# Performance work log

Hardware: AMD Instinct MI355X
Metric: run time of the kernel (lower is better)

The kernel has to match this reference:

```python
import jax, jax.numpy as jnp
import numpy as np

S, D, H = 4096, 2048, 16
HD = D // H

def setup_inputs() -> dict:
    key = jax.random.key(0)
    ks = jax.random.split(key, 9)
    s = 1.0 / np.sqrt(D)
    return {
        "hidden_states": jax.random.normal(ks[0], (S, D), jnp.float32),
        "Wq": jax.random.uniform(ks[1], (D, D), jnp.float32, -s, s),
        "bq": jax.random.uniform(ks[2], (D,), jnp.float32, -s, s),
        "Wk": jax.random.uniform(ks[3], (D, D), jnp.float32, -s, s),
        "bk": jax.random.uniform(ks[4], (D,), jnp.float32, -s, s),
        "Wv": jax.random.uniform(ks[5], (D, D), jnp.float32, -s, s),
        "bv": jax.random.uniform(ks[6], (D,), jnp.float32, -s, s),
        "Wo": jax.random.uniform(ks[7], (D, D), jnp.float32, -s, s),
        "bo": jax.random.uniform(ks[8], (D,), jnp.float32, -s, s),
    }

def reference(hidden_states, Wq, bq, Wk, bk, Wv, bv, Wo, bo):
    seq = hidden_states.shape[0]
    # projections (torch Linear: x @ W.T + b)
    q = (hidden_states @ Wq.T + bq).reshape(seq, H, HD).transpose(1, 0, 2)  # [H,S,hd]
    k = (hidden_states @ Wk.T + bk).reshape(seq, H, HD).transpose(1, 0, 2)
    v = (hidden_states @ Wv.T + bv).reshape(seq, H, HD).transpose(1, 0, 2)
    scale = 1.0 / np.sqrt(HD).astype(np.float32)
    qk = jnp.einsum('hqd,hkd->hqk', q, k) * scale  # [H,S,S]
    causal = jnp.tril(jnp.ones((seq, seq), bool))
    qk = jnp.where(causal, qk, -jnp.inf)
    attn = jax.nn.softmax(qk, axis=-1)
    out = jnp.einsum('hqk,hkd->hqd', attn, v)  # [H,S,hd]
    out = out.transpose(1, 0, 2).reshape(seq, D)
    return out @ Wo.T + bo
```

## Files before the change

### kernel.cpp

```cpp
#include <hip/hip_runtime.h>
#include <stdint.h>

#define S_LEN 4096
#define D_DIM 2048
#define NHEAD 16
#define HDIM  128

typedef short bf16x8 __attribute__((ext_vector_type(8)));
typedef float f32x4  __attribute__((ext_vector_type(4)));
typedef float f32x16 __attribute__((ext_vector_type(16)));

__device__ __forceinline__ unsigned short f2bf(float x) {
  union { float f; unsigned u; } v; v.f = x;
  unsigned r = v.u + 0x7FFFu + ((v.u >> 16) & 1u);
  return (unsigned short)(r >> 16);
}

__device__ __forceinline__ float bf2f(unsigned short s) {
  union { unsigned u; float f; } v; v.u = ((unsigned)s) << 16;
  return v.f;
}

__device__ __forceinline__ unsigned cvtpk_bf16(float lo, float hi_) {
  unsigned r;
  asm("v_cvt_pk_bf16_f32 %0, %1, %2" : "=v"(r) : "v"(lo), "v"(hi_));
  return r;
}

__device__ __forceinline__ void gload_lds16(const void* g, void* l) {
  __builtin_amdgcn_global_load_lds(
      (const __attribute__((address_space(1))) unsigned int*)g,
      (__attribute__((address_space(3))) unsigned int*)l, 16, 0, 0);
}

__global__ __launch_bounds__(256) void cvt_all(
    const float* __restrict__ X, const float* __restrict__ Wq,
    const float* __restrict__ Wk, const float* __restrict__ Wv,
    const float* __restrict__ Wo, unsigned short* __restrict__ out) {
  const size_t DD = (size_t)D_DIM * D_DIM;
  size_t i = ((size_t)blockIdx.x * 256 + threadIdx.x) * 8;
  const float* src; size_t off;
  if (i < 2 * DD)      { src = X;  off = i; }
  else if (i < 3 * DD) { src = Wq; off = i - 2 * DD; }
  else if (i < 4 * DD) { src = Wk; off = i - 3 * DD; }
  else if (i < 5 * DD) { src = Wv; off = i - 4 * DD; }
  else                 { src = Wo; off = i - 5 * DD; }
  float4 a = *(const float4*)(src + off);
  float4 b = *(const float4*)(src + off + 4);
  union { unsigned short s[8]; bf16x8 v; } o;
  o.s[0] = f2bf(a.x); o.s[1] = f2bf(a.y); o.s[2] = f2bf(a.z); o.s[3] = f2bf(a.w);
  o.s[4] = f2bf(b.x); o.s[5] = f2bf(b.y); o.s[6] = f2bf(b.z); o.s[7] = f2bf(b.w);
  *(bf16x8*)(out + i) = o.v;
}

__device__ __forceinline__ void stage256(
    const unsigned short* __restrict__ A, const unsigned short* __restrict__ W,
    unsigned short* la, unsigned short* lb, int m0, int n0, int k0,
    int wv, int lane) {
  const int K = 2048;
#pragma unroll
  for (int p = 0; p < 4; ++p) {
    const int off = wv * 1024 + p * 8192;
    const int o = off + lane * 16;
    const int half = o >> 14, rowh = (o >> 7) & 127, ch = (o >> 4) & 7;
    const int row = half * 128 + rowh;
    const int csrc = (ch ^ (rowh & 7)) * 8;
    gload_lds16(A + (size_t)(m0 + row) * K + k0 + csrc, la + (off >> 1));
    gload_lds16(W + (size_t)(n0 + row) * K + k0 + csrc, lb + (off >> 1));
  }
}

__global__ __launch_bounds__(512, 1) void gemm_qkv2(
    const unsigned short* __restrict__ A, const unsigned short* __restrict__ W,
    const float* __restrict__ bq, const float* __restrict__ bk,
    const float* __restrict__ bv, unsigned short* __restrict__ Q,
    unsigned short* __restrict__ Ko, unsigned short* __restrict__ V,
    float qsc) {
  __shared__ __attribute__((aligned(16))) unsigned short LA[2][16384];
  __shared__ __attribute__((aligned(16))) unsigned short LB[2][16384];
  const int m0 = blockIdx.y * 256, n0 = blockIdx.x * 256;
  const int tid = threadIdx.x, lane = tid & 63, wv = tid >> 6;
  const int wm = wv >> 2, wn = wv & 3;
  const int rA = lane & 15, g4 = lane >> 4;

  f32x4 acc[8][4];
#pragma unroll
  for (int i = 0; i < 8; ++i)
#pragma unroll
    for (int j = 0; j < 4; ++j)
#pragma unroll
      for (int r = 0; r < 4; ++r) acc[i][j][r] = 0.f;

  stage256(A, W, &LA[0][0], &LB[0][0], m0, n0, 0, wv, lane);
  stage256(A, W, &LA[1][0], &LB[1][0], m0, n0, 64, wv, lane);
  asm volatile("s_waitcnt vmcnt(8)" ::: "memory");
  __builtin_amdgcn_s_barrier();
  __builtin_amdgcn_sched_barrier(0);

  for (int t = 0; t < 32; ++t) {
    const unsigned short* la = &LA[t & 1][0] + wm * 8192;
    const unsigned short* lb = &LB[t & 1][0] + (wn >> 1) * 8192;
    const int rbB = (wn & 1) * 64;
#pragma unroll
    for (int kk = 0; kk < 2; ++kk) {
      bf16x8 af[8], bfv[4];
      const int sw = ((kk * 4 + g4) ^ (rA & 7)) * 8;
#pragma unroll
      for (int i = 0; i < 8; ++i)
        af[i] = *(const bf16x8*)(la + (i * 16 + rA) * 64 + sw);
#pragma unroll
      for (int j = 0; j < 4; ++j)
        bfv[j] = *(const bf16x8*)(lb + (rbB + j * 16 + rA) * 64 + sw);
      __builtin_amdgcn_s_setprio(1);
#pragma unroll
      for (int i = 0; i < 8; ++i)
#pragma unroll
        for (int j = 0; j < 4; ++j)
          acc[i][j] = __builtin_amdgcn_mfma_f32_16x16x32_bf16(af[i], bfv[j], acc[i][j], 0, 0, 0);
      __builtin_amdgcn_s_setprio(0);
    }
    if (t == 31) break;
    __builtin_amdgcn_s_barrier();
    __builtin_amdgcn_sched_barrier(0);
    if (t + 2 < 32) {
      stage256(A, W, &LA[t & 1][0], &LB[t & 1][0], m0, n0, (t + 2) * 64, wv, lane);
      asm volatile("s_waitcnt vmcnt(8)" ::: "memory");
    } else {
      asm volatile("s_waitcnt vmcnt(0)" ::: "memory");
    }
    __builtin_amdgcn_s_barrier();
    __builtin_amdgcn_sched_barrier(0);
  }

  const int cR = g4 * 4, cC = rA;
  const int seg = n0 >> 11;
  const float* bp = (seg == 0) ? bq : (seg == 1) ? bk : bv;
  unsigned short* op = (seg == 0) ? Q : (seg == 1) ? Ko : V;
  const float es = (seg == 0) ? qsc : 1.0f;
  const int ncl0 = (n0 & 2047) + wn * 64;
#pragma unroll
  for (int j = 0; j < 4; ++j) {
    const int col = ncl0 + j * 16 + cC;
    const float bvv = bp[col];
#pragma unroll
    for (int i = 0; i < 8; ++i) {
      const int row0 = m0 + wm * 128 + i * 16 + cR;
#pragma unroll
      for (int r = 0; r < 4; ++r)
        op[(size_t)(row0 + r) * D_DIM + col] = f2bf((acc[i][j][r] + bvv) * es);
    }
  }
}

__global__ __launch_bounds__(256, 2) void gemm_bt_f32(
    const unsigned short* __restrict__ A, const unsigned short* __restrict__ B,
    const float* __restrict__ bias, float* __restrict__ Cout,
    int M, int N, int K) {
  __shared__ __attribute__((aligned(16))) unsigned short As[128 * 32];
  __shared__ __attribute__((aligned(16))) unsigned short Bs[128 * 32];
  const int m0 = blockIdx.y * 128, n0 = blockIdx.x * 128;
  const int tid = threadIdx.x, lane = tid & 63, wv = tid >> 6;
  const int wm = wv >> 1, wn = wv & 1;
  const int rA = lane & 15, kb = (lane >> 4) * 8;

  f32x4 acc[4][4];
#pragma unroll
  for (int i = 0; i < 4; ++i)
#pragma unroll
    for (int j = 0; j < 4; ++j)
#pragma unroll
      for (int r = 0; r < 4; ++r) acc[i][j][r] = 0.f;

  for (int k0 = 0; k0 < K; k0 += 32) {
    __syncthreads();
#pragma unroll
    for (int p = 0; p < 2; ++p) {
      const int rr = (wv * 2 + p) * 16 + (lane >> 2);
      const int cc = lane & 3;
      gload_lds16(A + (size_t)(m0 + rr) * K + k0 + cc * 8, As + (wv * 2 + p) * 512);
      gload_lds16(B + (size_t)(n0 + rr) * K + k0 + cc * 8, Bs + (wv * 2 + p) * 512);
    }
    __syncthreads();
    bf16x8 af[4], bfr[4];
#pragma unroll
    for (int i = 0; i < 4; ++i)
      af[i] = *(const bf16x8*)(As + (wm * 64 + i * 16 + rA) * 32 + kb);
#pragma unroll
    for (int j = 0; j < 4; ++j)
      bfr[j] = *(const bf16x8*)(Bs + (wn * 64 + j * 16 + rA) * 32 + kb);
#pragma unroll
    for (int i = 0; i < 4; ++i)
#pragma unroll
      for (int j = 0; j < 4; ++j)
        acc[i][j] = __builtin_amdgcn_mfma_f32_16x16x32_bf16(af[i], bfr[j], acc[i][j], 0, 0, 0);
  }

  const int cR = (lane >> 4) * 4, cC = lane & 15;
#pragma unroll
  for (int j = 0; j < 4; ++j) {
    const int col = n0 + wn * 64 + j * 16 + cC;
    const float bvv = bias[col];
#pragma unroll
    for (int i = 0; i < 4; ++i) {
      const int row0 = m0 + wm * 64 + i * 16 + cR;
#pragma unroll
      for (int r = 0; r < 4; ++r)
        Cout[(size_t)(row0 + r) * N + col] = acc[i][j][r] + bvv;
    }
  }
}

__global__ __launch_bounds__(256, 2) void attn_part(
    const unsigned short* __restrict__ Qb, const unsigned short* __restrict__ Kb,
    const unsigned short* __restrict__ Vb, unsigned short* __restrict__ Opart,
    float* __restrict__ ML) {
  __shared__ __attribute__((aligned(16))) unsigned short Ks[64 * 128];
  __shared__ __attribute__((aligned(16))) unsigned short Vt[128 * 64];
  const int bid = blockIdx.x;
  const int h  = ((bid & 7) << 1) | ((bid >> 3) & 1);
  const int hf = (bid >> 4) & 1;
  const int qi = 31 - (bid >> 5);
  const int q0 = qi * 128;
  const int u2 = (h * 32 + qi) * 2 + hf;
  const int tid = threadIdx.x, lane = tid & 63, wv = tid >> 6;
  const int qc = lane & 31, hi = lane >> 5;
  const int q0w = q0 + wv * 32;
  const int myq = q0w + qc;
  const int kp = tid & 31, hb = (tid >> 5) * 16;

  bf16x8 qf[8];
#pragma unroll
  for (int sl = 0; sl < 8; ++sl)
    qf[sl] = *(const bf16x8*)(Qb + (size_t)myq * D_DIM + h * HDIM + sl * 16 + hi * 8);

  f32x16 oacc[4];
#pragma unroll
  for (int nf = 0; nf < 4; ++nf)
#pragma unroll
    for (int r = 0; r < 16; ++r) oacc[nf][r] = 0.f;
  float mh = -3.0e38f, l = 0.f;

  const int klo = hf * (qi + 1), khi = klo + qi + 1;
  const int wqmax = q0w + 31;

  for (int kt = klo; kt < khi; ++kt) {
    const int k0 = kt * 64;
    __syncthreads();
#pragma unroll
    for (int p = 0; p < 4; ++p) {
      const int ob = wv * 4096 + p * 1024;
      const int o = ob + lane * 16;
      const int r = o >> 8, c = (o >> 4) & 15;
      gload_lds16(Kb + (size_t)(k0 + r) * D_DIM + h * HDIM + (c ^ (r & 7)) * 8,
                  Ks + ob / 2);
    }
    {
      const unsigned short* s0 = Vb + (size_t)(k0 + 2 * kp) * D_DIM + h * HDIM + hb;
      union { uint4 u[4]; unsigned short s[32]; } t;
      t.u[0] = *(const uint4*)s0;           t.u[1] = *(const uint4*)(s0 + 8);
      t.u[2] = *(const uint4*)(s0 + D_DIM); t.u[3] = *(const uint4*)(s0 + D_DIM + 8);
#pragma unroll
      for (int w = 0; w < 16; ++w) {
        const int hd = hb + w;
        const unsigned val = (unsigned)t.s[w] | ((unsigned)t.s[16 + w] << 16);
        *(unsigned*)((char*)Vt + hd * 128 + (((kp >> 2) ^ (hd & 7)) << 4) + ((kp & 3) << 2)) = val;
      }
    }
    __syncthreads();
    if (k0 > wqmax) continue;

    f32x16 sacc[2];
#pragma unroll
    for (int kb = 0; kb < 2; ++kb)
#pragma unroll
      for (int r = 0; r < 16; ++r) sacc[kb][r] = 0.f;
    __builtin_amdgcn_s_setprio(1);
#pragma unroll
    for (int sl = 0; sl < 8; ++sl) {
#pragma unroll
      for (int kb = 0; kb < 2; ++kb) {
        const int row = kb * 32 + qc;
        bf16x8 kfr = *(const bf16x8*)((const char*)Ks + row * 256 +
                                      (((2 * sl + hi) ^ (qc & 7)) << 4));
        sacc[kb] = __builtin_amdgcn_mfma_f32_32x32x16_bf16(kfr, qf[sl], sacc[kb], 0, 0, 0);
      }
    }
    __builtin_amdgcn_s_setprio(0);

    const bool needmask = (k0 + 63 > q0w);
    if (needmask) {
      const int dq = myq - k0;
#pragma unroll
      for (int kb = 0; kb < 2; ++kb)
#pragma unroll
        for (int r = 0; r < 16; ++r) {
          const int kk = kb * 32 + (r & 3) + 8 * (r >> 2) + 4 * hi;
          if (kk > dq) sacc[kb][r] = -3.0e38f;
        }
    }
    float mx0[8];
#pragma unroll
    for (int t = 0; t < 8; ++t)
      mx0[t] = fmaxf(fmaxf(sacc[0][t], sacc[0][t + 8]),
                     fmaxf(sacc[1][t], sacc[1][t + 8]));
    float mx = fmaxf(fmaxf(fmaxf(mx0[0], mx0[1]), fmaxf(mx0[2], mx0[3])),
                     fmaxf(fmaxf(mx0[4], mx0[5]), fmaxf(mx0[6], mx0[7])));
    mx = fmaxf(mx, __shfl_xor(mx, 32));
    if (!__all(mx <= mh + 11.5f)) {
      const float mnew = fmaxf(mh, mx);
      const float corr = exp2f(mh - mnew);
      mh = mnew;
      l *= corr;
#pragma unroll
      for (int r = 0; r < 16; ++r) {
        const float cr = __shfl(corr, (r & 3) + 8 * (r >> 2) + 4 * hi);
#pragma unroll
        for (int nf = 0; nf < 4; ++nf) oacc[nf][r] *= cr;
      }
    }
    float rs = 0.f;
#pragma unroll
    for (int kb = 0; kb < 2; ++kb)
#pragma unroll
      for (int r = 0; r < 16; ++r) {
        const float p = exp2f(sacc[kb][r] - mh);
        sacc[kb][r] = p;
        rs += p;
      }
    rs += __shfl_xor(rs, 32);
    l += rs;

    bf16x8 pa[4];
#pragma unroll
    for (int kb = 0; kb < 2; ++kb)
#pragma unroll
      for (int s = 0; s < 2; ++s) {
        const int b = s * 8;
        unsigned pk0 = cvtpk_bf16(sacc[kb][b + 0], sacc[kb][b + 1]);
        unsigned pk1 = cvtpk_bf16(sacc[kb][b + 2], sacc[kb][b + 3]);
        unsigned pk2 = cvtpk_bf16(sacc[kb][b + 4], sacc[kb][b + 5]);
        unsigned pk3 = cvtpk_bf16(sacc[kb][b + 6], sacc[kb][b + 7]);
        const unsigned sw0 = (unsigned)__shfl_xor((int)pk0, 32);
        const unsigned sw1 = (unsigned)__shfl_xor((int)pk1, 32);
        const unsigned sw2 = (unsigned)__shfl_xor((int)pk2, 32);
        const unsigned sw3 = (unsigned)__shfl_xor((int)pk3, 32);
        union { unsigned u[4]; bf16x8 v; } f;
        if (hi) { f.u[0] = sw2; f.u[1] = sw3; f.u[2] = pk2; f.u[3] = pk3; }
        else    { f.u[0] = pk0; f.u[1] = pk1; f.u[2] = sw0; f.u[3] = sw1; }
        pa[kb * 2 + s] = f.v;
      }

    __builtin_amdgcn_s_setprio(1);
#pragma unroll
    for (int nf = 0; nf < 4; ++nf) {
      const int hd = 32 * nf + qc;
#pragma unroll
      for (int ks = 0; ks < 4; ++ks) {
        bf16x8 vf = *(const bf16x8*)((const char*)Vt + hd * 128 +
                                     (((2 * ks + hi) ^ (qc & 7)) << 4));
        oacc[nf] = __builtin_amdgcn_mfma_f32_32x32x16_bf16(pa[ks], vf, oacc[nf], 0, 0, 0);
      }
    }
    __builtin_amdgcn_s_setprio(0);
  }

  unsigned short* ob = Opart + (size_t)u2 * 16384;
#pragma unroll
  for (int r = 0; r < 16; ++r) {
    const int rl = wv * 32 + (r & 3) + 8 * (r >> 2) + 4 * hi;
#pragma unroll
    for (int nf = 0; nf < 4; ++nf)
      ob[rl * 128 + 32 * nf + qc] = f2bf(oacc[nf][r]);
  }
  if (hi == 0) {
    ML[(size_t)u2 * 256 + wv * 32 + qc] = mh;
    ML[(size_t)u2 * 256 + 128 + wv * 32 + qc] = l;
  }
}

__global__ __launch_bounds__(256) void attn_combine(
    const unsigned short* __restrict__ Opart, const float* __restrict__ ML,
    unsigned short* __restrict__ Ob) {
  const int u = blockIdx.x;
  const int h = u >> 5, qi = u & 31;
  const int tid = threadIdx.x;
  const int row = tid >> 1, c0 = (tid & 1) * 64;
  const float m1 = ML[(size_t)(u * 2 + 0) * 256 + row];
  const float l1 = ML[(size_t)(u * 2 + 0) * 256 + 128 + row];
  const float m2 = ML[(size_t)(u * 2 + 1) * 256 + row];
  const float l2 = ML[(size_t)(u * 2 + 1) * 256 + 128 + row];
  const float M  = fmaxf(m1, m2);
  const float a1 = exp2f(m1 - M), a2 = exp2f(m2 - M);
  const float inv = 1.f / (a1 * l1 + a2 * l2);
  const unsigned short* p1 = Opart + (size_t)(u * 2 + 0) * 16384 + row * 128 + c0;
  const unsigned short* p2 = Opart + (size_t)(u * 2 + 1) * 16384 + row * 128 + c0;
  unsigned short* o = Ob + (size_t)(qi * 128 + row) * D_DIM + h * HDIM + c0;
#pragma unroll
  for (int c = 0; c < 64; c += 8) {
    bf16x8 v1 = *(const bf16x8*)(p1 + c);
    bf16x8 v2 = *(const bf16x8*)(p2 + c);
    union { unsigned short s[8]; bf16x8 v; } out;
#pragma unroll
    for (int e = 0; e < 8; ++e)
      out.s[e] = f2bf((bf2f((unsigned short)v1[e]) * a1 +
                       bf2f((unsigned short)v2[e]) * a2) * inv);
    *(bf16x8*)(o + c) = out.v;
  }
}

extern "C" void kernel_launch(void* const* d_in, const int* in_sizes, int n_in,
                              void* d_out, int out_size, void* d_ws, size_t ws_size,
                              hipStream_t stream) {
  const float* X  = (const float*)d_in[0];
  const float* Wq = (const float*)d_in[1];
  const float* bq = (const float*)d_in[2];
  const float* Wk = (const float*)d_in[3];
  const float* bk = (const float*)d_in[4];
  const float* Wv = (const float*)d_in[5];
  const float* bv = (const float*)d_in[6];
  const float* Wo = (const float*)d_in[7];
  const float* bo = (const float*)d_in[8];
  float* out = (float*)d_out;

  unsigned short* ws = (unsigned short*)d_ws;
  const size_t SD = (size_t)S_LEN * D_DIM;
  const size_t DD = (size_t)D_DIM * D_DIM;
  unsigned short* Xb  = ws;
  unsigned short* Wqb = Xb + SD;
  unsigned short* Wob = Wqb + 3 * DD;
  unsigned short* Qb  = Wob + DD;
  unsigned short* Kb  = Qb + SD;
  unsigned short* Vb  = Kb + SD;
  unsigned short* AOb = Vb + SD;
  unsigned short* Opart = ws;
  float* ML = (float*)(ws + SD + 2 * DD);

  cvt_all<<<(int)(6 * DD / 8 / 256), 256, 0, stream>>>(X, Wq, Wk, Wv, Wo, Xb);

  const float qsc = 0.08838834764831845f * 1.4426950408889634f;
  gemm_qkv2<<<dim3(24, 16), 512, 0, stream>>>(Xb, Wqb, bq, bk, bv, Qb, Kb, Vb, qsc);

  attn_part<<<dim3(1024), 256, 0, stream>>>(Qb, Kb, Vb, Opart, ML);
  attn_combine<<<dim3(512), 256, 0, stream>>>(Opart, ML, AOb);

  gemm_bt_f32<<<dim3(16, 32), 256, 0, stream>>>(AOb, Wob, bo, out, S_LEN, D_DIM, D_DIM);
}
```

Measured before the change: 336.9 us.

## Restructure QKV GEMM into 8-phase pipeline with half-tile staging and block swizzle

Replaces the two-barrier-per-K-step QKV GEMM loop with an 8-phase schedule. Each phase loads its LDS fragments for one quadrant of the 256x256 tile, issues one half-tile global-to-LDS stage, then runs 16 MFMAs, so global loads are spread evenly across the compute. The warp-to-tile mapping changes so each wave owns scattered 64x32 quadrants, and the epilogue indexing is updated to match. Blocks are also remapped from a 2D grid through a 1D swizzle that groups neighbouring tiles, aiming for better L2 reuse across CUs. The cost is more barriers per K step and more intricate vmcnt bookkeeping, which risks stalls or subtle ordering errors.

```diff
diff --git a/kernel.cpp b/kernel.cpp
--- a/kernel.cpp
+++ b/kernel.cpp
@@ -53,24 +53,71 @@
   *(bf16x8*)(out + i) = o.v;
 }
 
-__device__ __forceinline__ void stage256(
+__device__ __forceinline__ void stage_half(
+    const unsigned short* __restrict__ src, unsigned short* lds,
+    int rc0, int t, int h, int wv, int lane) {
+#pragma unroll
+  for (int p = 0; p < 2; ++p) {
+    const int off = wv * 2048 + p * 1024;
+    const int o = off + lane * 16;
+    const int row = o >> 7, ch = (o >> 4) & 7;
+    gload_lds16(src + (size_t)(rc0 + h * 128 + row) * 2048 + t * 64 + ((ch ^ (row & 7)) << 3),
+                lds + h * 8192 + (off >> 1));
+  }
+}
+
+template<int PA, int PB>
+__device__ __forceinline__ void phase(
+    f32x4 (&acc)[8][4], const unsigned short* Abuf, const unsigned short* Bbuf,
     const unsigned short* __restrict__ A, const unsigned short* __restrict__ W,
-    unsigned short* la, unsigned short* lb, int m0, int n0, int k0,
-    int wv, int lane) {
-  const int K = 2048;
-#pragma unroll
-  for (int p = 0; p < 4; ++p) {
-    const int off = wv * 1024 + p * 8192;
-    const int o = off + lane * 16;
-    const int half = o >> 14, rowh = (o >> 7) & 127, ch = (o >> 4) & 7;
-    const int row = half * 128 + rowh;
-    const int csrc = (ch ^ (rowh & 7)) * 8;
-    gload_lds16(A + (size_t)(m0 + row) * K + k0 + csrc, la + (off >> 1));
-    gload_lds16(W + (size_t)(n0 + row) * K + k0 + csrc, lb + (off >> 1));
-  }
-}
-
-__global__ __launch_bounds__(512, 1) void gemm_qkv2(
+    unsigned short* stLA, unsigned short* stLB,
+    int m0, int n0, int sm, int sh, int stT, int vm,
+    int wm, int wn, int rA, int g4, int wv, int lane) {
+  const unsigned short* Ab = Abuf + PA * 8192;
+  const unsigned short* Bb = Bbuf + PB * 8192;
+  bf16x8 af0[4], af1[4], bf0[2], bf1[2];
+  const int s0 = (g4 ^ (rA & 7)) << 3, s1 = ((4 + g4) ^ (rA & 7)) << 3;
+#pragma unroll
+  for (int i = 0; i < 4; ++i) {
+    const int rr = (wm * 64 + i * 16 + rA) * 64;
+    af0[i] = *(const bf16x8*)(Ab + rr + s0);
+    af1[i] = *(const bf16x8*)(Ab + rr + s1);
+  }
+#pragma unroll
+  for (int j = 0; j < 2; ++j) {
+    const int rr = (wn * 32 + j * 16 + rA) * 64;
+    bf0[j] = *(const bf16x8*)(Bb + rr + s0);
+    bf1[j] = *(const bf16x8*)(Bb + rr + s1);
+  }
+  if (stT < 32) {
+    if (sm == 0) stage_half(A, stLA, m0, stT, sh, wv, lane);
+    else         stage_half(W, stLB, n0, stT, sh, wv, lane);
+  }
+  __builtin_amdgcn_s_barrier();
+  asm volatile("s_waitcnt lgkmcnt(0)" ::: "memory");
+  __builtin_amdgcn_sched_barrier(0);
+  __builtin_amdgcn_s_setprio(1);
+#pragma unroll
+  for (int i = 0; i < 4; ++i)
+#pragma unroll
+    for (int j = 0; j < 2; ++j)
+      acc[PA * 4 + i][PB * 2 + j] =
+          __builtin_amdgcn_mfma_f32_16x16x32_bf16(af0[i], bf0[j], acc[PA * 4 + i][PB * 2 + j], 0, 0, 0);
+#pragma unroll
+  for (int i = 0; i < 4; ++i)
+#pragma unroll
+    for (int j = 0; j < 2; ++j)
+      acc[PA * 4 + i][PB * 2 + j] =
+          __builtin_amdgcn_mfma_f32_16x16x32_bf16(af1[i], bf1[j], acc[PA * 4 + i][PB * 2 + j], 0, 0, 0);
+  __builtin_amdgcn_s_setprio(0);
+  if (vm == 1) asm volatile("s_waitcnt vmcnt(4)" ::: "memory");
+  if (vm == 2) asm volatile("s_waitcnt vmcnt(0)" ::: "memory");
+  __builtin_amdgcn_s_barrier();
+  __builtin_amdgcn_sched_barrier(0);
+  asm volatile("" ::: "memory");
+}
+
+__global__ __launch_bounds__(512, 1) void gemm_qkv8(
     const unsigned short* __restrict__ A, const unsigned short* __restrict__ W,
     const float* __restrict__ bq, const float* __restrict__ bk,
     const float* __restrict__ bv, unsigned short* __restrict__ Q,
@@ -78,7 +125,9 @@
     float qsc) {
   __shared__ __attribute__((aligned(16))) unsigned short LA[2][16384];
   __shared__ __attribute__((aligned(16))) unsigned short LB[2][16384];
-  const int m0 = blockIdx.y * 256, n0 = blockIdx.x * 256;
+  const int bid = blockIdx.x;
+  const int swz = (bid & 7) * 48 + (bid >> 3);
+  const int m0 = (swz / 24) * 256, n0 = (swz % 24) * 256;
   const int tid = threadIdx.x, lane = tid & 63, wv = tid >> 6;
   const int wm = wv >> 2, wn = wv & 3;
   const int rA = lane & 15, g4 = lane >> 4;
@@ -91,63 +140,45 @@
 #pragma unroll
       for (int r = 0; r < 4; ++r) acc[i][j][r] = 0.f;
 
-  stage256(A, W, &LA[0][0], &LB[0][0], m0, n0, 0, wv, lane);
-  stage256(A, W, &LA[1][0], &LB[1][0], m0, n0, 64, wv, lane);
-  asm volatile("s_waitcnt vmcnt(8)" ::: "memory");
+  stage_half(A, &LA[0][0], m0, 0, 0, wv, lane);
+  stage_half(W, &LB[0][0], n0, 0, 0, wv, lane);
+  stage_half(A, &LA[0][0], m0, 0, 1, wv, lane);
+  stage_half(W, &LB[0][0], n0, 0, 1, wv, lane);
+  stage_half(A, &LA[1][0], m0, 1, 0, wv, lane);
+  stage_half(W, &LB[1][0], n0, 1, 0, wv, lane);
+  asm volatile("s_waitcnt vmcnt(4)" ::: "memory");
   __builtin_amdgcn_s_barrier();
   __builtin_amdgcn_sched_barrier(0);
 
-  for (int t = 0; t < 32; ++t) {
-    const unsigned short* la = &LA[t & 1][0] + wm * 8192;
-    const unsigned short* lb = &LB[t & 1][0] + (wn >> 1) * 8192;
-    const int rbB = (wn & 1) * 64;
-#pragma unroll
-    for (int kk = 0; kk < 2; ++kk) {
-      bf16x8 af[8], bfv[4];
-      const int sw = ((kk * 4 + g4) ^ (rA & 7)) * 8;
-#pragma unroll
-      for (int i = 0; i < 8; ++i)
-        af[i] = *(const bf16x8*)(la + (i * 16 + rA) * 64 + sw);
-#pragma unroll
-      for (int j = 0; j < 4; ++j)
-        bfv[j] = *(const bf16x8*)(lb + (rbB + j * 16 + rA) * 64 + sw);
-      __builtin_amdgcn_s_setprio(1);
-#pragma unroll
-      for (int i = 0; i < 8; ++i)
-#pragma unroll
-        for (int j = 0; j < 4; ++j)
-          acc[i][j] = __builtin_amdgcn_mfma_f32_16x16x32_bf16(af[i], bfv[j], acc[i][j], 0, 0, 0);
-      __builtin_amdgcn_s_setprio(0);
-    }
-    if (t == 31) break;
-    __builtin_amdgcn_s_barrier();
-    __builtin_amdgcn_sched_barrier(0);
-    if (t + 2 < 32) {
-      stage256(A, W, &LA[t & 1][0], &LB[t & 1][0], m0, n0, (t + 2) * 64, wv, lane);
-      asm volatile("s_waitcnt vmcnt(8)" ::: "memory");
-    } else {
-      asm volatile("s_waitcnt vmcnt(0)" ::: "memory");
-    }
-    __builtin_amdgcn_s_barrier();
-    __builtin_amdgcn_sched_barrier(0);
-  }
-
-  const int cR = g4 * 4, cC = rA;
+  for (int i = 0; i < 16; ++i) {
+    const int t1 = 2 * i + 1, t2 = 2 * i + 2, t3 = 2 * i + 3;
+    const int vm4 = (i == 15) ? 2 : 1;
+    const int vm8 = (i == 15) ? 0 : 1;
+    phase<0, 0>(acc, &LA[0][0], &LB[0][0], A, W, &LA[1][0], &LB[1][0], m0, n0, 0, 1, t1, 0, wm, wn, rA, g4, wv, lane);
+    phase<0, 1>(acc, &LA[0][0], &LB[0][0], A, W, &LA[1][0], &LB[1][0], m0, n0, 1, 1, t1, 0, wm, wn, rA, g4, wv, lane);
+    phase<1, 0>(acc, &LA[0][0], &LB[0][0], A, W, &LA[0][0], &LB[0][0], m0, n0, 0, 0, t2, 0, wm, wn, rA, g4, wv, lane);
+    phase<1, 1>(acc, &LA[0][0], &LB[0][0], A, W, &LA[0][0], &LB[0][0], m0, n0, 1, 0, t2, vm4, wm, wn, rA, g4, wv, lane);
+    phase<0, 0>(acc, &LA[1][0], &LB[1][0], A, W, &LA[0][0], &LB[0][0], m0, n0, 0, 1, t2, 0, wm, wn, rA, g4, wv, lane);
+    phase<0, 1>(acc, &LA[1][0], &LB[1][0], A, W, &LA[0][0], &LB[0][0], m0, n0, 1, 1, t2, 0, wm, wn, rA, g4, wv, lane);
+    phase<1, 0>(acc, &LA[1][0], &LB[1][0], A, W, &LA[1][0], &LB[1][0], m0, n0, 0, 0, t3, 0, wm, wn, rA, g4, wv, lane);
+    phase<1, 1>(acc, &LA[1][0], &LB[1][0], A, W, &LA[1][0], &LB[1][0], m0, n0, 1, 0, t3, vm8, wm, wn, rA, g4, wv, lane);
+  }
+
   const int seg = n0 >> 11;
   const float* bp = (seg == 0) ? bq : (seg == 1) ? bk : bv;
   unsigned short* op = (seg == 0) ? Q : (seg == 1) ? Ko : V;
   const float es = (seg == 0) ? qsc : 1.0f;
-  const int ncl0 = (n0 & 2047) + wn * 64;
-#pragma unroll
-  for (int j = 0; j < 4; ++j) {
-    const int col = ncl0 + j * 16 + cC;
-    const float bvv = bp[col];
-#pragma unroll
-    for (int i = 0; i < 8; ++i) {
-      const int row0 = m0 + wm * 128 + i * 16 + cR;
+  const int cR = g4 * 4, cC = rA;
+#pragma unroll
+  for (int J = 0; J < 4; ++J) {
+    const int cl = (n0 & 2047) + (J >> 1) * 128 + wn * 32 + (J & 1) * 16 + cC;
+    const float bvv = bp[cl];
+#pragma unroll
+    for (int I = 0; I < 8; ++I) {
+      const int row0 = m0 + (I >> 2) * 128 + wm * 64 + (I & 3) * 16 + cR;
 #pragma unroll
       for (int r = 0; r < 4; ++r)
-        op[(size_t)(row0 + r) * D_DIM + col] = f2bf((acc[i][j][r] + bvv) * es);
+        op[(size_t)(row0 + r) * D_DIM + cl] = f2bf((acc[I][J][r] + bvv) * es);
     }
   }
 }
@@ -438,7 +469,7 @@
   cvt_all<<<(int)(6 * DD / 8 / 256), 256, 0, stream>>>(X, Wq, Wk, Wv, Wo, Xb);
 
   const float qsc = 0.08838834764831845f * 1.4426950408889634f;
-  gemm_qkv2<<<dim3(24, 16), 512, 0, stream>>>(Xb, Wqb, bq, bk, bv, Qb, Kb, Vb, qsc);
+  gemm_qkv8<<<dim3(384), 512, 0, stream>>>(Xb, Wqb, bq, bk, bv, Qb, Kb, Vb, qsc);
 
   attn_part<<<dim3(1024), 256, 0, stream>>>(Qb, Kb, Vb, Opart, ML);
   attn_combine<<<dim3(512), 256, 0, stream>>>(Opart, ML, AOb);
```

New measurement: 355.8 us. +5.6%, slower.
